# Kernel tuning notes

Hardware: AMD Instinct MI355X
Metric: run time of the kernel (lower is better)

## Reference

```python
import jax, jax.numpy as jnp
import numpy as np

B, N, C, D = 8, 8192, 3, 64
S, K = 2048, 32
EPS = 1e-7       # acos clamp epsilon (matches torch code)
BN_EPS = 1e-5    # torch BatchNorm2d default eps


def _safe_unit(v):
    # v: [..., C]; returns (v/||v|| with 0 where ||v||==0, ||v||).
    # Matches torch's `u[u != u] = 0` NaN fix and has zero grad at v==0.
    sq = jnp.sum(v * v, axis=-1, keepdims=True)
    d = jnp.where(sq > 0, jnp.sqrt(jnp.where(sq > 0, sq, 1.0)), 0.0)
    u = jnp.where(d > 0, v / jnp.where(d > 0, d, 1.0), 0.0)
    return u, d


def _acos_clamped(x):
    return jnp.arccos(jnp.clip(x, -1.0 + EPS, 1.0 - EPS))


def _conv_bn_relu(x, w, b, gamma, beta):
    # x: [B, Cin, K, S]; w: [Cout, Cin] (1x1 Conv2d); BN in training mode (batch stats).
    y = jnp.einsum('oc,bcks->boks', w, x) + b[None, :, None, None]
    mean = jnp.mean(y, axis=(0, 2, 3), keepdims=True)
    var = jnp.mean((y - mean) ** 2, axis=(0, 2, 3), keepdims=True)
    y = (y - mean) / jnp.sqrt(var + BN_EPS)
    y = y * gamma[None, :, None, None] + beta[None, :, None, None]
    return jax.nn.relu(y)


def _forward(contour, LOA, feature_maps,
             fe_w1, fe_b1, fe_g1, fe_be1, fe_w2, fe_b2, fe_g2, fe_be2,
             fl_w1, fl_b1, fl_g1, fl_be1, fl_w2, fl_b2, fl_g2, fl_be2):
    # --- downsampling: uniform linspace indices (torch .long() truncates) ---
    new_index = jnp.linspace(0.0, N - 1, S).astype(jnp.int32)               # [S]
    sampled = contour[:, new_index, :]                                       # [B,S,C]
    new_LOA = LOA[:, new_index, :]                                           # [B,S,C]
    # --- contiguous circular neighborhoods around each sampled index ---
    group_idx = (new_index[:, None] - K // 2 + jnp.arange(K)[None, :]) % N   # [S,K]
    # --- irregular gathers ---
    nb_pts = contour[:, group_idx, :]                                        # [B,S,K,C]
    nb_loa = LOA[:, group_idx, :]                                            # [B,S,K,C]
    local = nb_pts - sampled[:, :, None, :]                                  # [B,S,K,C]
    d1_unit, d1 = _safe_unit(local)
    axis = new_LOA[:, :, None, :]                                            # [B,S,1,C]
    a1 = jnp.sum(d1_unit * axis, axis=-1, keepdims=True)
    a2 = jnp.sum(d1_unit * nb_loa, axis=-1, keepdims=True)
    a3 = _acos_clamped(jnp.sum(nb_loa * axis, axis=-1, keepdims=True))
    # NOTE: torch does `D_0[D_0 == 0] = -1` on a *bool* tensor; bool(-1) is True,
    # so D_0 becomes all-True and D_0.float()*a3 == a3 (sign is always +1).
    inner_vec = local - jnp.roll(local, 1, axis=2)
    inner_unit, _ = _safe_unit(inner_vec)
    a4 = jnp.sum(inner_unit * nb_loa, axis=-1, keepdims=True)
    a5 = jnp.sum(inner_unit * jnp.roll(nb_loa, 1, axis=2), axis=-1, keepdims=True)
    a6 = _acos_clamped(jnp.sum(nb_loa * jnp.roll(nb_loa, 1, axis=2), axis=-1, keepdims=True))
    # same bool-assignment quirk for D_1 -> a6 unchanged
    d2 = _acos_clamped(jnp.sum(d1_unit * jnp.roll(d1_unit, 1, axis=2), axis=-1, keepdims=True))
    rif = jnp.concatenate([d1, d2, a1, a2, a3, a4, a5, a6], axis=-1)         # [B,S,K,8]
    # --- feature enhancement MLP on [B, ch, K, S] layout ---
    x = jnp.transpose(rif, (0, 3, 2, 1))                                     # [B,8,K,S]
    x = _conv_bn_relu(x, fe_w1, fe_b1, fe_g1, fe_be1)                        # [B,32,K,S]
    x = _conv_bn_relu(x, fe_w2, fe_b2, fe_g2, fe_be2)                        # [B,64,K,S]
    # --- gather input feature maps with the same indices, concat channels ---
    fmap = jnp.transpose(feature_maps, (0, 2, 1))                            # [B,N,D]
    grouped = jnp.transpose(fmap[:, group_idx, :], (0, 3, 2, 1))             # [B,D,K,S]
    x = jnp.concatenate([x, grouped], axis=1)                                # [B,128,K,S]
    # --- filter MLP + max over neighborhood ---
    x = _conv_bn_relu(x, fl_w1, fl_b1, fl_g1, fl_be1)                        # [B,128,K,S]
    x = _conv_bn_relu(x, fl_w2, fl_b2, fl_g2, fl_be2)                        # [B,256,K,S]
    out = jnp.max(x, axis=2)                                                 # [B,256,S]
    return sampled, new_LOA, out


def setup_inputs() -> dict:
    key = jax.random.key(0)
    ks = jax.random.split(key, 12)

    def w(k, o, i):
        return jax.random.normal(k, (o, i), jnp.float32) / np.sqrt(i)

    return {
        'contour': jax.random.normal(ks[0], (B, N, C), jnp.float32),
        'LOA': jax.random.normal(ks[1], (B, N, C), jnp.float32),
        'feature_maps': jax.random.normal(ks[2], (B, D, N), jnp.float32),
        'fe_w1': w(ks[3], 32, 8),  'fe_b1': jnp.zeros(32),
        'fe_g1': jnp.ones(32),     'fe_be1': jnp.zeros(32),
        'fe_w2': w(ks[4], 64, 32), 'fe_b2': jnp.zeros(64),
        'fe_g2': jnp.ones(64),     'fe_be2': jnp.zeros(64),
        'fl_w1': w(ks[5], 128, 128), 'fl_b1': jnp.zeros(128),
        'fl_g1': jnp.ones(128),      'fl_be1': jnp.zeros(128),
        'fl_w2': w(ks[6], 256, 128), 'fl_b2': jnp.zeros(256),
        'fl_g2': jnp.ones(256),      'fl_be2': jnp.zeros(256),
    }


def reference(contour, LOA, feature_maps,
              fe_w1, fe_b1, fe_g1, fe_be1, fe_w2, fe_b2, fe_g2, fe_be2,
              fl_w1, fl_b1, fl_g1, fl_be1, fl_w2, fl_b2, fl_g2, fl_be2):
    return _forward(contour, LOA, feature_maps,
                    fe_w1, fe_b1, fe_g1, fe_be1, fe_w2, fe_b2, fe_g2, fe_be2,
                    fl_w1, fl_b1, fl_g1, fl_be1, fl_w2, fl_b2, fl_g2, fl_be2)
```

## Files before the change

kernel.cpp:

```cpp
#include <hip/hip_runtime.h>
#include <stdint.h>

#define NPTS 8192
#define SSZ  2048
#define QTOT (8*2048*32)

#define F_MOM1   4
#define F_MOM2   12
#define F_SC1    972
#define F_SH1    1004
#define F_SC2    1036
#define F_SH2    1100
#define F_SC3    1164
#define F_SH3    1292
#define F_SC4    1420
#define F_SH4    1676
#define F_WF1    1932
#define F_WF2    2188
#define F_G1     53388
#define F_BE1    53420
#define F_G2     53452
#define F_BE2    53516
#define F_G3     53580
#define F_BE3    53708
#define F_G4     53836
#define F_BE4    54092
#define F_M1     57344
#define F_M2     57376
#define F_P      60000
#define F_S3P    77000
#define F_C4P    94000
#define CTR_OFF  524288ull
#define LOA_OFF  1310720ull
#define U3H_OFF  2097152ull
#define U3L_OFF  2129920ull
#define U4H_OFF  2162688ull
#define U4L_OFF  2228224ull
#define U2H_OFF  2293760ull
#define U2L_OFF  2297856ull
#define Y3_OFF   2301952ull
#define WS_T1    (2301952ull + 134217728ull)

typedef __attribute__((ext_vector_type(8))) short s8v;
typedef __attribute__((ext_vector_type(4))) short s4v;
typedef __attribute__((ext_vector_type(4))) float f4v;
typedef __attribute__((ext_vector_type(4))) float fl4;
#define MFMA(a,b,c) __builtin_amdgcn_mfma_f32_16x16x32_bf16(a,b,c,0,0,0)

__device__ inline float bf2f(unsigned short u){ return __uint_as_float(((uint32_t)u)<<16); }
__device__ inline unsigned short f2bf(float f){
    uint32_t x=__float_as_uint(f);
    return (unsigned short)((x + 0x7fffu + ((x>>16)&1u))>>16);
}
__device__ inline float clipf(float x){
    const float LO=(float)(-1.0+1e-7), HI=(float)(1.0-1e-7);
    return fminf(fmaxf(x,LO),HI);
}
__device__ inline float wredsum(float v){
#pragma unroll
    for(int m=1;m<64;m<<=1) v+=__shfl_xor(v,m,64);
    return v;
}
__device__ inline float ldin(const void* p,size_t i,int md){
    return md ? ((const float*)p)[i] : bf2f(((const unsigned short*)p)[i]);
}
__device__ inline int sidx(int s){ return (s*8191)/2047; }

__global__ void k_detect(const void* contour,int* flag){
    __shared__ int he;
    if(threadIdx.x==0) he=0;
    __syncthreads();
    const unsigned short* u=(const unsigned short*)contour;
    int h=0;
    for(int i=threadIdx.x;i<4096;i+=256){
        unsigned short lo=u[2*i];
        if(((lo>>7)&0xFF)>=0x86) h++;
    }
    atomicAdd(&he,h);
    __syncthreads();
    if(threadIdx.x==0) *flag = (he>400) ? 1 : 0;
}

__global__ __launch_bounds__(256) void k_convert(
    const void* ctr,const void* loa,
    const void* w1,const void* w2,const void* w3,const void* w4,
    const void* g1,const void* be1,const void* g2,const void* be2,
    const void* g3,const void* be3,const void* g4,const void* be4,
    float* F, float* ctrf, float* loaf,
    unsigned short* u2h, unsigned short* u2l,
    unsigned short* u3h, unsigned short* u3l,
    unsigned short* u4h, unsigned short* u4l,
    float* out)
{
    int md=((const int*)F)[0];
    int i = blockIdx.x*256+threadIdx.x;
    ctrf[i]=ldin(ctr,i,md);
    loaf[i]=ldin(loa,i,md);
    if(i<16384){
        int b=i>>11, s=i&2047;
        int idx=sidx(s);
        size_t cb=((size_t)b*NPTS+idx)*3;
        size_t ob=(size_t)i*3;
        out[ob]        =ldin(ctr,cb  ,md);
        out[ob+1]      =ldin(ctr,cb+1,md);
        out[ob+2]      =ldin(ctr,cb+2,md);
        out[49152+ob]  =ldin(loa,cb  ,md);
        out[49152+ob+1]=ldin(loa,cb+1,md);
        out[49152+ob+2]=ldin(loa,cb+2,md);
    }
    if(i<256)  F[F_WF1+i]=ldin(w1,i,md);
    if(i<2048) F[F_WF2+i]=ldin(w2,i,md);
    if(i<2048){
        int j=i&7, lane=(i>>3)&63, mt=i>>9;
        int m=lane&15, kk=((lane>>4)<<3)|j;
        float w=ldin(w2,(size_t)(mt*16+m)*32 + kk, md);
        unsigned short hi=f2bf(w);
        u2h[i]=hi; u2l[i]=f2bf(w-bf2f(hi));
    }
    if(i<16384){
        int j=i&7, lane=(i>>3)&63, kt=(i>>9)&3, mt=i>>11;
        int m=lane&15, kk=((lane>>4)<<3)|j;
        float w=ldin(w3,(size_t)(mt*16+m)*128 + kt*32+kk, md);
        unsigned short hi=f2bf(w);
        u3h[i]=hi; u3l[i]=f2bf(w-bf2f(hi));
    }
    if(i<32768){
        int j=i&7, lane=(i>>3)&63, kt=(i>>9)&3, mt=i>>11;
        int m=lane&15, kk=((lane>>4)<<3)|j;
        float w=ldin(w4,(size_t)(mt*16+m)*128 + kt*32+kk, md);
        unsigned short hi=f2bf(w);
        u4h[i]=hi; u4l[i]=f2bf(w-bf2f(hi));
    }
    if(i<968)   F[4+i]=0.f;
    if(i<16896) F[F_P+i]=0.f;
    if(i<16384) F[F_S3P+i]=0.f;
    if(i<32768) F[F_C4P+i]=0.f;
    if(i<32){ F[F_G1+i]=ldin(g1,i,md); F[F_BE1+i]=ldin(be1,i,md); }
    if(i<64){ F[F_G2+i]=ldin(g2,i,md); F[F_BE2+i]=ldin(be2,i,md); }
    if(i<128){ F[F_G3+i]=ldin(g3,i,md); F[F_BE3+i]=ldin(be3,i,md); }
    if(i<256){ F[F_G4+i]=ldin(g4,i,md); F[F_BE4+i]=ldin(be4,i,md); }
}

__device__ inline void rif_compute(const float* __restrict__ ctr,const float* __restrict__ loa,
                                   int b,int s,int k,float r[8])
{
    int idx=sidx(s);
    int gi=(idx-16+k)&(NPTS-1);
    size_t cb=((size_t)b*NPTS+gi)*3;
    float px=ctr[cb],py=ctr[cb+1],pz=ctr[cb+2];
    float lx=loa[cb],ly=loa[cb+1],lz=loa[cb+2];
    float sx=__shfl(px,16,32),sy=__shfl(py,16,32),sz=__shfl(pz,16,32);
    float ax=__shfl(lx,16,32),ay=__shfl(ly,16,32),az=__shfl(lz,16,32);
    float vx=px-sx,vy=py-sy,vz=pz-sz;
    float sq=vx*vx+vy*vy+vz*vz;
    float d1=sq>0.f?sqrtf(sq):0.f;
    float inv=d1>0.f?1.f/d1:0.f;
    float ux=vx*inv,uy=vy*inv,uz=vz*inv;
    float a1=ux*ax+uy*ay+uz*az;
    float a2=ux*lx+uy*ly+uz*lz;
    float a3=acosf(clipf(lx*ax+ly*ay+lz*az));
    int src=(k+31)&31;
    float pvx=__shfl(vx,src,32),pvy=__shfl(vy,src,32),pvz=__shfl(vz,src,32);
    float plx=__shfl(lx,src,32),ply=__shfl(ly,src,32),plz=__shfl(lz,src,32);
    float pux=__shfl(ux,src,32),puy=__shfl(uy,src,32),puz=__shfl(uz,src,32);
    float ivx=vx-pvx,ivy=vy-pvy,ivz=vz-pvz;
    float isq=ivx*ivx+ivy*ivy+ivz*ivz;
    float idn=isq>0.f?1.f/sqrtf(isq):0.f;
    float iux=ivx*idn,iuy=ivy*idn,iuz=ivz*idn;
    float a4=iux*lx+iuy*ly+iuz*lz;
    float a5=iux*plx+iuy*ply+iuz*plz;
    float a6=acosf(clipf(lx*plx+ly*ply+lz*plz));
    float d2=acosf(clipf(ux*pux+uy*puy+uz*puz));
    r[0]=d1;r[1]=d2;r[2]=a1;r[3]=a2;r[4]=a3;r[5]=a4;r[6]=a5;r[7]=a6;
}

__global__ __launch_bounds__(256) void k_features(
    const float* __restrict__ ctrf,const float* __restrict__ loaf,
    float* __restrict__ mom1,float* __restrict__ mom2)
{
    __shared__ float sm1[8],sm2[64];
    int t=threadIdx.x;
    if(t<8)sm1[t]=0.f;
    if(t<64)sm2[t]=0.f;
    __syncthreads();
    int lane=t&63,k=t&31;
    int q=blockIdx.x*256+t;
    int pos=q>>5,b=pos>>11,s=pos&2047;
    float r[8];
    rif_compute(ctrf,loaf,b,s,k,r);
#pragma unroll
    for(int i=0;i<8;i++){ float sv=wredsum(r[i]); if(lane==0)atomicAdd(&sm1[i],sv); }
#pragma unroll
    for(int i=0;i<8;i++)
#pragma unroll
        for(int j=i;j<8;j++){ float sv=wredsum(r[i]*r[j]); if(lane==0)atomicAdd(&sm2[i*8+j],sv); }
    __syncthreads();
    if(t<8)atomicAdd(&mom1[t],sm1[t]);
    if(t<64)atomicAdd(&mom2[t],sm2[t]);
}

__global__ void k_bn1(float* F){
    int o=threadIdx.x;
    if(o>=32)return;
    const float invP=1.0f/(float)QTOT;
    float m[8],w[8];
#pragma unroll
    for(int c=0;c<8;c++){ m[c]=F[F_MOM1+c]*invP; w[c]=F[F_WF1+o*8+c]; }
    float Ey=0.f;
#pragma unroll
    for(int c=0;c<8;c++) Ey+=w[c]*m[c];
    float Eyy=0.f;
#pragma unroll
    for(int i=0;i<8;i++)
#pragma unroll
        for(int j=0;j<8;j++){
            int a=i<j?i:j,bb=i<j?j:i;
            Eyy+=w[i]*w[j]*F[F_MOM2+a*8+bb]*invP;
        }
    float var=fmaxf(Eyy-Ey*Ey,0.f);
    float sc=F[F_G1+o]/sqrtf(var+1e-5f);
    F[F_SC1+o]=sc;
    F[F_SH1+o]=F[F_BE1+o]-Ey*sc;
}

#define S2T 264
__global__ __launch_bounds__(256) void k_stats2m(
    const float* __restrict__ ctrf,const float* __restrict__ loaf,
    const float* __restrict__ F,float* __restrict__ P)
{
    __shared__ unsigned short TH[32*S2T];
    __shared__ unsigned short TL[32*S2T];
    int t=threadIdx.x, wv=t>>6, lane=t&63;
    int quad=lane>>4, col=lane&15;
    int mi=wv>>1, ni=wv&1;
    float acc8[8];
#pragma unroll
    for(int k=0;k<8;k++) acc8[k]=0.f;
    f4v Z; Z[0]=0.f;Z[1]=0.f;Z[2]=0.f;Z[3]=0.f;
    f4v C0=Z, C1=Z;
    const float* wf1=F+F_WF1;
    const float* sc1=F+F_SC1; const float* sh1=F+F_SH1;
    for(int tt=0;tt<2;++tt){
        int tile=blockIdx.x*2+tt;
        int pos=tile*8 + wv*2 + (lane>>5);
        int b=pos>>11, s=pos&2047;
        float r[8]; rif_compute(ctrf,loaf,b,s,lane&31,r);
        int mypos=wv*64+lane;
#pragma unroll
        for(int c=0;c<32;c++){
            const float* w=wf1+c*8;
            float y=w[0]*r[0]+w[1]*r[1]+w[2]*r[2]+w[3]*r[3]
                   +w[4]*r[4]+w[5]*r[5]+w[6]*r[6]+w[7]*r[7];
            float h=fmaxf(y*sc1[c]+sh1[c],0.f);
            unsigned short hi=f2bf(h);
            TH[c*S2T+mypos]=hi;
            TL[c*S2T+mypos]=f2bf(h-bf2f(hi));
        }
        __syncthreads();
#pragma unroll
        for(int kt=0;kt<8;kt++){
            s8v AH=*(const s8v*)(TH+(mi*16+col)*S2T + kt*32 + quad*8);
            s8v AL=*(const s8v*)(TL+(mi*16+col)*S2T + kt*32 + quad*8);
            s8v BH=*(const s8v*)(TH+(ni*16+col)*S2T + kt*32 + quad*8);
            s8v BL=*(const s8v*)(TL+(ni*16+col)*S2T + kt*32 + quad*8);
            if(kt&1){
                C1=MFMA(AH,BH,C1); C1=MFMA(AH,BL,C1); C1=MFMA(AL,BH,C1);
            }else{
                C0=MFMA(AH,BH,C0); C0=MFMA(AH,BL,C0); C0=MFMA(AL,BH,C0);
            }
        }
#pragma unroll
        for(int k=0;k<8;k++){
            int c=wv*8+k;
            const unsigned short* ph=TH+c*S2T+lane*4;
            const unsigned short* pl=TL+c*S2T+lane*4;
            acc8[k]+=bf2f(ph[0])+bf2f(ph[1])+bf2f(ph[2])+bf2f(ph[3])
                    +bf2f(pl[0])+bf2f(pl[1])+bf2f(pl[2])+bf2f(pl[3]);
        }
        __syncthreads();
    }
    float* Ps=P+(size_t)(blockIdx.x&15)*1056;
#pragma unroll
    for(int rg=0;rg<4;rg++){
        float v=C0[rg]+C1[rg];
        atomicAdd(&Ps[32+(mi*16+quad*4+rg)*32 + ni*16+col], v);
    }
#pragma unroll
    for(int k=0;k<8;k++){
        float sv=wredsum(acc8[k]);
        if(lane==0) atomicAdd(&Ps[wv*8+k],sv);
    }
}

__global__ void k_red(float* F){
    int t=threadIdx.x;
    for(int e=t;e<1056;e+=256){
        float s=0.f;
#pragma unroll
        for(int k=0;k<16;k++) s+=F[F_P+k*1056+e];
        if(e<32) F[F_M1+e]=s; else F[F_M2+e-32]=s;
    }
    __syncthreads();
    int o=t;
    if(o<64){
        const float invP=1.0f/(float)QTOT;
        const float* w=F+F_WF2+o*32;
        const float* M2=F+F_M2;
        float Ey=0.f;
#pragma unroll
        for(int c=0;c<32;c++) Ey+=w[c]*F[F_M1+c];
        Ey*=invP;
        float Eyy=0.f;
        for(int c1=0;c1<32;c1++){
            float acc=0.f;
#pragma unroll
            for(int c2=0;c2<32;c2++) acc+=w[c2]*M2[c1*32+c2];
            Eyy+=w[c1]*acc;
        }
        Eyy*=invP;
        float var=fmaxf(Eyy-Ey*Ey,0.f);
        float s=F[F_G2+o]/sqrtf(var+1e-5f);
        F[F_SC2+o]=s;
        F[F_SH2+o]=F[F_BE2+o]-Ey*s;
    }
}

__global__ void k_bnd3(float* F){
    int o=threadIdx.x;
    if(o>=128)return;
    float sum=0.f,ssq=0.f;
    for(int s=0;s<64;s++){
        sum+=F[F_S3P+s*256+o];
        ssq+=F[F_S3P+s*256+128+o];
    }
    const float invP=1.0f/(float)QTOT;
    float mean=sum*invP;
    float var=fmaxf(ssq*invP-mean*mean,0.f);
    float sc=F[F_G3+o]/sqrtf(var+1e-5f);
    F[F_SC3+o]=sc;
    F[F_SH3+o]=F[F_BE3+o]-mean*sc;
}

__global__ void k_bnd4(float* F){
    int o=threadIdx.x;
    if(o>=256)return;
    float sum=0.f,ssq=0.f;
    for(int s=0;s<64;s++){
        sum+=F[F_C4P+s*512+o];
        ssq+=F[F_C4P+s*512+256+o];
    }
    const float invP=1.0f/(float)QTOT;
    float mean=sum*invP;
    float var=fmaxf(ssq*invP-mean*mean,0.f);
    float sc=F[F_G4+o]/sqrtf(var+1e-5f);
    F[F_SC4+o]=sc;
    F[F_SH4+o]=F[F_BE4+o]-mean*sc;
}

#define XST 136

__device__ inline void build_x2_8(
    const float* __restrict__ ctrf,const float* __restrict__ loaf,
    const void* __restrict__ fm,const float* __restrict__ F,
    const unsigned short* __restrict__ u2h,const unsigned short* __restrict__ u2l,
    int md,int b,int s0,int wv,int lane,
    unsigned short* XH,unsigned short* XL)
{
    int quad=lane>>4, col=lane&15;
    if(wv<4){
        float r8[8]; rif_compute(ctrf,loaf,b,s0+(lane>>5),lane&31,r8);
        const float* wf1=F+F_WF1;
        const float* sc1=F+F_SC1; const float* sh1=F+F_SH1;
        s8v vh,vl;
#pragma unroll
        for(int j=0;j<8;j++){
            int o=8*wv+j;
            const float* w=wf1+o*8;
            float y=w[0]*r8[0]+w[1]*r8[1]+w[2]*r8[2]+w[3]*r8[3]
                   +w[4]*r8[4]+w[5]*r8[5]+w[6]*r8[6]+w[7]*r8[7];
            float h=fmaxf(y*sc1[o]+sh1[o],0.f);
            unsigned short hi=f2bf(h);
            vh[j]=(short)hi;
            vl[j]=(short)f2bf(h-bf2f(hi));
        }
        *(s8v*)(XH + lane*XST + 8*wv)=vh;
        *(s8v*)(XL + lane*XST + 8*wv)=vl;
    }else{
        int dbase=16*(wv-4);
        int s=s0+(lane>>5), k=lane&31;
        int gi=(sidx(s)-16+k)&(NPTS-1);
        size_t fb=(size_t)b*64*NPTS+gi;
        for(int g=0;g<2;g++){
            s8v vh,vl;
#pragma unroll
            for(int j=0;j<8;j++){
                int d=dbase+g*8+j;
                float v = md ? ((const float*)fm)[fb+(size_t)d*NPTS]
                             : bf2f(((const unsigned short*)fm)[fb+(size_t)d*NPTS]);
                unsigned short hi=f2bf(v);
                vh[j]=(short)hi;
                vl[j]=(short)f2bf(v-bf2f(hi));
            }
            *(s8v*)(XH + lane*XST + 64 + dbase + g*8)=vh;
            *(s8v*)(XL + lane*XST + 64 + dbase + g*8)=vl;
        }
    }
    __syncthreads();
    int cg=wv>>1, nb=(wv&1)*2;
    s8v AH=*(const s8v*)(u2h+(cg*64+lane)*8);
    s8v AL=*(const s8v*)(u2l+(cg*64+lane)*8);
    s8v BH0=*(const s8v*)(XH+((nb  )*16+col)*XST+quad*8);
    s8v BL0=*(const s8v*)(XL+((nb  )*16+col)*XST+quad*8);
    s8v BH1=*(const s8v*)(XH+((nb+1)*16+col)*XST+quad*8);
    s8v BL1=*(const s8v*)(XL+((nb+1)*16+col)*XST+quad*8);
    f4v Z; Z[0]=0.f;Z[1]=0.f;Z[2]=0.f;Z[3]=0.f;
    f4v c0=MFMA(AH,BH0,Z), c1=MFMA(AH,BH1,Z);
    c0=MFMA(AH,BL0,c0); c1=MFMA(AH,BL1,c1);
    c0=MFMA(AL,BH0,c0); c1=MFMA(AL,BH1,c1);
    __syncthreads();
    const float* sc2=F+F_SC2; const float* sh2=F+F_SH2;
    int chb=cg*16+quad*4;
    float g0=sc2[chb],g1=sc2[chb+1],g2=sc2[chb+2],g3=sc2[chb+3];
    float b0=sh2[chb],b1=sh2[chb+1],b2=sh2[chb+2],b3=sh2[chb+3];
#pragma unroll
    for(int i=0;i<2;i++){
        f4v c = i? c1 : c0;
        int p=(nb+i)*16+col;
        float v0=fmaxf(c[0]*g0+b0,0.f);
        float v1=fmaxf(c[1]*g1+b1,0.f);
        float v2=fmaxf(c[2]*g2+b2,0.f);
        float v3=fmaxf(c[3]*g3+b3,0.f);
        unsigned short h0=f2bf(v0),h1=f2bf(v1),h2=f2bf(v2),h3=f2bf(v3);
        s4v vh,vl;
        vh[0]=(short)h0; vh[1]=(short)h1; vh[2]=(short)h2; vh[3]=(short)h3;
        vl[0]=(short)f2bf(v0-bf2f(h0)); vl[1]=(short)f2bf(v1-bf2f(h1));
        vl[2]=(short)f2bf(v2-bf2f(h2)); vl[3]=(short)f2bf(v3-bf2f(h3));
        *(s4v*)(XH + p*XST + chb)=vh;
        *(s4v*)(XL + p*XST + chb)=vl;
    }
}

#define G1_STEP8(UH,UL) \
    for(int kt=0;kt<4;kt++){ \
        s8v BH[4],BL[4]; \
        for(int nt=0;nt<4;nt++){ \
            int boff=(nt*16+col)*XST + kt*32 + quad*8; \
            BH[nt]=*(const s8v*)(XH+boff); \
            BL[nt]=*(const s8v*)(XL+boff); \
        } \
        { \
            s8v AH=*(const s8v*)(UH+((wv*4+kt)*64+lane)*8); \
            s8v AL=*(const s8v*)(UL+((wv*4+kt)*64+lane)*8); \
            for(int nt=0;nt<4;nt++) C[nt]=MFMA(AH,BH[nt],C[nt]); \
            for(int nt=0;nt<4;nt++) C[nt]=MFMA(AH,BL[nt],C[nt]); \
            for(int nt=0;nt<4;nt++) C[nt]=MFMA(AL,BH[nt],C[nt]); \
        } \
    }

#define G2_STEP8(UH,UL) \
    for(int kt=0;kt<4;kt++){ \
        s8v BH[4],BL[4]; \
        for(int nt=0;nt<4;nt++){ \
            int boff=(nt*16+col)*XST + kt*32 + quad*8; \
            BH[nt]=*(const s8v*)(XH+boff); \
            BL[nt]=*(const s8v*)(XL+boff); \
        } \
        for(int mi=0;mi<2;mi++){ \
            int mt=2*wv+mi; \
            s8v AH=*(const s8v*)(UH+((mt*4+kt)*64+lane)*8); \
            s8v AL=*(const s8v*)(UL+((mt*4+kt)*64+lane)*8); \
            for(int nt=0;nt<4;nt++) C2[mi][nt]=MFMA(AH,BH[nt],C2[mi][nt]); \
            for(int nt=0;nt<4;nt++) C2[mi][nt]=MFMA(AH,BL[nt],C2[mi][nt]); \
            for(int nt=0;nt<4;nt++) C2[mi][nt]=MFMA(AL,BH[nt],C2[mi][nt]); \
        } \
    }

__global__ __launch_bounds__(512) void k_stats3(
    const float* __restrict__ ctrf,const float* __restrict__ loaf,
    const void* __restrict__ fm,float* __restrict__ F,
    const unsigned short* __restrict__ u2h,const unsigned short* __restrict__ u2l,
    const unsigned short* __restrict__ u3h,const unsigned short* __restrict__ u3l,
    unsigned short* __restrict__ y3)
{
    __shared__ unsigned short XH[64*XST];
    __shared__ unsigned short XL[64*XST];
    __shared__ float as_[128],qs_[128];
    int t=threadIdx.x, wv=t>>6, lane=t&63;
    if(t<128){as_[t]=0.f;qs_[t]=0.f;}
    int md=((const int*)F)[0];
    int pos0=blockIdx.x*2, b=pos0>>11, s0=pos0&2047;
    build_x2_8(ctrf,loaf,fm,F,u2h,u2l,md,b,s0,wv,lane,XH,XL);
    __syncthreads();
    int quad=lane>>4, col=lane&15;
    f4v Z; Z[0]=0.f;Z[1]=0.f;Z[2]=0.f;Z[3]=0.f;
    f4v C[4];
#pragma unroll
    for(int nt=0;nt<4;nt++) C[nt]=Z;
#pragma unroll
    G1_STEP8(u3h,u3l)
    if(y3){
#pragma unroll
        for(int nt=0;nt<4;nt++){
            s4v v4;
#pragma unroll
            for(int rg=0;rg<4;rg++) v4[rg]=(short)f2bf(C[nt][rg]);
            *(s4v*)(y3 + (size_t)blockIdx.x*8192 + (size_t)(wv*4+nt)*256 + lane*4) = v4;
        }
    }
#pragma unroll
    for(int rg=0;rg<4;rg++){
        float sm=0.f,sq=0.f;
#pragma unroll
        for(int nt=0;nt<4;nt++){ float v=C[nt][rg]; sm+=v; sq+=v*v; }
        sm+=__shfl_xor(sm,1); sq+=__shfl_xor(sq,1);
        sm+=__shfl_xor(sm,2); sq+=__shfl_xor(sq,2);
        sm+=__shfl_xor(sm,4); sq+=__shfl_xor(sq,4);
        sm+=__shfl_xor(sm,8); sq+=__shfl_xor(sq,8);
        if(col==0){
            int ch=wv*16+quad*4+rg;
            atomicAdd(&as_[ch],sm); atomicAdd(&qs_[ch],sq);
        }
    }
    __syncthreads();
    float* Ps=F+F_S3P+(size_t)(blockIdx.x&63)*256;
    if(t<128){atomicAdd(&Ps[t],as_[t]);atomicAdd(&Ps[128+t],qs_[t]);}
}

__global__ __launch_bounds__(512) void k_conv4y(
    float* __restrict__ F,
    const unsigned short* __restrict__ u4h,const unsigned short* __restrict__ u4l,
    const unsigned short* __restrict__ y3,
    float* __restrict__ maxb)
{
    __shared__ unsigned short XH[64*XST];
    __shared__ unsigned short XL[64*XST];
    __shared__ float as_[256],qs_[256];
    int t=threadIdx.x, wv=t>>6, lane=t&63;
    if(t<256){as_[t]=0.f; qs_[t]=0.f;}
    int quad=lane>>4, col=lane&15;
    int pos0=blockIdx.x*2, b=pos0>>11, s0=pos0&2047;
    const float* sc3=F+F_SC3; const float* sh3=F+F_SH3;
    {
        int chb=wv*16+quad*4;
#pragma unroll
        for(int nt=0;nt<4;nt++){
            s4v v4=*(const s4v*)(y3 + (size_t)blockIdx.x*8192 + (size_t)(wv*4+nt)*256 + lane*4);
            s4v vh,vl;
#pragma unroll
            for(int rg=0;rg<4;rg++){
                float v=bf2f((unsigned short)v4[rg]);
                v=fmaxf(v*sc3[chb+rg]+sh3[chb+rg],0.f);
                unsigned short hi=f2bf(v);
                vh[rg]=(short)hi;
                vl[rg]=(short)f2bf(v-bf2f(hi));
            }
            int p=nt*16+col;
            *(s4v*)(XH + p*XST + chb)=vh;
            *(s4v*)(XL + p*XST + chb)=vl;
        }
    }
    __syncthreads();
    f4v Z; Z[0]=0.f;Z[1]=0.f;Z[2]=0.f;Z[3]=0.f;
    f4v C2[2][4];
#pragma unroll
    for(int mi=0;mi<2;mi++)
#pragma unroll
        for(int nt=0;nt<4;nt++) C2[mi][nt]=Z;
#pragma unroll
    G2_STEP8(u4h,u4l)
#pragma unroll
    for(int mi=0;mi<2;mi++){
        int mt=2*wv+mi;
#pragma unroll
        for(int rg=0;rg<4;rg++){
            float sm=0.f,sq=0.f,mx0=-3.4e38f,mx1=-3.4e38f;
#pragma unroll
            for(int nt=0;nt<4;nt++){
                float v=C2[mi][nt][rg];
                sm+=v; sq+=v*v;
                if(nt<2) mx0=fmaxf(mx0,v); else mx1=fmaxf(mx1,v);
            }
            sm+=__shfl_xor(sm,1); sq+=__shfl_xor(sq,1);
            sm+=__shfl_xor(sm,2); sq+=__shfl_xor(sq,2);
            sm+=__shfl_xor(sm,4); sq+=__shfl_xor(sq,4);
            sm+=__shfl_xor(sm,8); sq+=__shfl_xor(sq,8);
            mx0=fmaxf(mx0,__shfl_xor(mx0,1)); mx1=fmaxf(mx1,__shfl_xor(mx1,1));
            mx0=fmaxf(mx0,__shfl_xor(mx0,2)); mx1=fmaxf(mx1,__shfl_xor(mx1,2));
            mx0=fmaxf(mx0,__shfl_xor(mx0,4)); mx1=fmaxf(mx1,__shfl_xor(mx1,4));
            mx0=fmaxf(mx0,__shfl_xor(mx0,8)); mx1=fmaxf(mx1,__shfl_xor(mx1,8));
            if(col==0){
                int ch=mt*16+quad*4+rg;
                atomicAdd(&as_[ch],sm); atomicAdd(&qs_[ch],sq);
                size_t ob=((size_t)b*256+ch)*SSZ + s0;
                maxb[ob]=mx0; maxb[ob+1]=mx1;
            }
        }
    }
    __syncthreads();
    float* Ps=F+F_C4P+(size_t)(blockIdx.x&63)*512;
    if(t<256){atomicAdd(&Ps[t],as_[t]);atomicAdd(&Ps[256+t],qs_[t]);}
}

__global__ __launch_bounds__(512) void k_conv4(
    const float* __restrict__ ctrf,const float* __restrict__ loaf,
    const void* __restrict__ fm,float* __restrict__ F,
    const unsigned short* __restrict__ u2h,const unsigned short* __restrict__ u2l,
    const unsigned short* __restrict__ u3h,const unsigned short* __restrict__ u3l,
    const unsigned short* __restrict__ u4h,const unsigned short* __restrict__ u4l,
    float* __restrict__ maxb)
{
    __shared__ unsigned short XH[64*XST];
    __shared__ unsigned short XL[64*XST];
    __shared__ float as_[256],qs_[256];
    int t=threadIdx.x, wv=t>>6, lane=t&63;
    if(t<256){as_[t]=0.f; qs_[t]=0.f;}
    int md=((const int*)F)[0];
    int pos0=blockIdx.x*2, b=pos0>>11, s0=pos0&2047;
    build_x2_8(ctrf,loaf,fm,F,u2h,u2l,md,b,s0,wv,lane,XH,XL);
    __syncthreads();
    int quad=lane>>4, col=lane&15;
    f4v Z; Z[0]=0.f;Z[1]=0.f;Z[2]=0.f;Z[3]=0.f;
    f4v C[4];
#pragma unroll
    for(int nt=0;nt<4;nt++) C[nt]=Z;
#pragma unroll
    G1_STEP8(u3h,u3l)
    __syncthreads();
    const float* sc3=F+F_SC3; const float* sh3=F+F_SH3;
    {
        int chb=wv*16+quad*4;
#pragma unroll
        for(int nt=0;nt<4;nt++){
            int p=nt*16+col;
            s4v vh,vl;
#pragma unroll
            for(int rg=0;rg<4;rg++){
                float v=C[nt][rg];
                v=fmaxf(v*sc3[chb+rg]+sh3[chb+rg],0.f);
                unsigned short hi=f2bf(v);
                vh[rg]=(short)hi;
                vl[rg]=(short)f2bf(v-bf2f(hi));
            }
            *(s4v*)(XH + p*XST + chb)=vh;
            *(s4v*)(XL + p*XST + chb)=vl;
        }
    }
    __syncthreads();
    f4v C2[2][4];
#pragma unroll
    for(int mi=0;mi<2;mi++)
#pragma unroll
        for(int nt=0;nt<4;nt++) C2[mi][nt]=Z;
#pragma unroll
    G2_STEP8(u4h,u4l)
#pragma unroll
    for(int mi=0;mi<2;mi++){
        int mt=2*wv+mi;
#pragma unroll
        for(int rg=0;rg<4;rg++){
            float sm=0.f,sq=0.f,mx0=-3.4e38f,mx1=-3.4e38f;
#pragma unroll
            for(int nt=0;nt<4;nt++){
                float v=C2[mi][nt][rg];
                sm+=v; sq+=v*v;
                if(nt<2) mx0=fmaxf(mx0,v); else mx1=fmaxf(mx1,v);
            }
            sm+=__shfl_xor(sm,1); sq+=__shfl_xor(sq,1);
            sm+=__shfl_xor(sm,2); sq+=__shfl_xor(sq,2);
            sm+=__shfl_xor(sm,4); sq+=__shfl_xor(sq,4);
            sm+=__shfl_xor(sm,8); sq+=__shfl_xor(sq,8);
            mx0=fmaxf(mx0,__shfl_xor(mx0,1)); mx1=fmaxf(mx1,__shfl_xor(mx1,1));
            mx0=fmaxf(mx0,__shfl_xor(mx0,2)); mx1=fmaxf(mx1,__shfl_xor(mx1,2));
            mx0=fmaxf(mx0,__shfl_xor(mx0,4)); mx1=fmaxf(mx1,__shfl_xor(mx1,4));
            mx0=fmaxf(mx0,__shfl_xor(mx0,8)); mx1=fmaxf(mx1,__shfl_xor(mx1,8));
            if(col==0){
                int ch=mt*16+quad*4+rg;
                atomicAdd(&as_[ch],sm); atomicAdd(&qs_[ch],sq);
                size_t ob=((size_t)b*256+ch)*SSZ + s0;
                maxb[ob]=mx0; maxb[ob+1]=mx1;
            }
        }
    }
    __syncthreads();
    float* Ps=F+F_C4P+(size_t)(blockIdx.x&63)*512;
    if(t<256){atomicAdd(&Ps[t],as_[t]);atomicAdd(&Ps[256+t],qs_[t]);}
}

__global__ __launch_bounds__(256) void k_apply(
    const float* __restrict__ F,float* __restrict__ out)
{
    int e4=blockIdx.x*256+threadIdx.x;
    int j=(e4>>9)&255;
    float sc=F[F_SC4+j],sh=F[F_SH4+j];
    fl4* p=(fl4*)(out+98304)+e4;
    fl4 v=*p;
    v[0]=fmaxf(v[0]*sc+sh,0.f);
    v[1]=fmaxf(v[1]*sc+sh,0.f);
    v[2]=fmaxf(v[2]*sc+sh,0.f);
    v[3]=fmaxf(v[3]*sc+sh,0.f);
    *p=v;
}

extern "C" void kernel_launch(void* const* d_in, const int* in_sizes, int n_in,
                              void* d_out, int out_size, void* d_ws, size_t ws_size,
                              hipStream_t stream)
{
    const void* contour=d_in[0];
    const void* loa    =d_in[1];
    const void* fm     =d_in[2];
    const void* w1 =d_in[3];  const void* g1 =d_in[5];  const void* be1=d_in[6];
    const void* w2 =d_in[7];  const void* g2 =d_in[9];  const void* be2=d_in[10];
    const void* w3 =d_in[11]; const void* g3 =d_in[13]; const void* be3=d_in[14];
    const void* w4 =d_in[15]; const void* g4 =d_in[17]; const void* be4=d_in[18];
    float* out=(float*)d_out;

    float* F=(float*)d_ws;
    char* base=(char*)d_ws;
    float* ctrf=(float*)(base+CTR_OFF);
    float* loaf=(float*)(base+LOA_OFF);
    unsigned short* u3h=(unsigned short*)(base+U3H_OFF);
    unsigned short* u3l=(unsigned short*)(base+U3L_OFF);
    unsigned short* u4h=(unsigned short*)(base+U4H_OFF);
    unsigned short* u4l=(unsigned short*)(base+U4L_OFF);
    unsigned short* u2h=(unsigned short*)(base+U2H_OFF);
    unsigned short* u2l=(unsigned short*)(base+U2L_OFF);
    int tier = (ws_size >= WS_T1) ? 1 : 0;
    unsigned short* y3 = tier==1 ? (unsigned short*)(base+Y3_OFF) : (unsigned short*)0;
    float* maxb=out+98304;

    k_detect<<<1,256,0,stream>>>(contour,(int*)d_ws);
    k_convert<<<768,256,0,stream>>>(contour,loa,w1,w2,w3,w4,g1,be1,g2,be2,g3,be3,g4,be4,
                                    F,ctrf,loaf,u2h,u2l,u3h,u3l,u4h,u4l,out);
    k_features<<<2048,256,0,stream>>>(ctrf,loaf,F+F_MOM1,F+F_MOM2);
    k_bn1<<<1,32,0,stream>>>(F);
    k_stats2m<<<1024,256,0,stream>>>(ctrf,loaf,F,F+F_P);
    k_red<<<1,256,0,stream>>>(F);
    k_stats3<<<8192,512,0,stream>>>(ctrf,loaf,fm,F,u2h,u2l,u3h,u3l,y3);
    k_bnd3<<<1,128,0,stream>>>(F);
    if(tier==1){
        k_conv4y<<<8192,512,0,stream>>>(F,u4h,u4l,y3,maxb);
    }else{
        k_conv4<<<8192,512,0,stream>>>(ctrf,loaf,fm,F,u2h,u2l,u3h,u3l,u4h,u4l,maxb);
    }
    k_bnd4<<<1,256,0,stream>>>(F);
    k_apply<<<4096,256,0,stream>>>(F,out);
}
```

Measured before the change: 591.5 us.

## Cache per-neighbor geometric features in workspace and reuse across stats kernels

k_features now writes its 8 per-neighbor rotation-invariant features into a workspace buffer when the workspace is large enough. k_stats2m and a new k_stats3r variant read that buffer instead of recomputing the acos-heavy features, so the trigonometry runs once instead of three times. The cost is 16 MB of extra writes and reads, and this path only runs when the workspace exceeds the new tier threshold.

After: 531.3 us. -10.2%, faster.

```diff
diff --git a/kernel.cpp b/kernel.cpp
--- a/kernel.cpp
+++ b/kernel.cpp
@@ -40,6 +40,8 @@
 #define U2L_OFF  2297856ull
 #define Y3_OFF   2301952ull
 #define WS_T1    (2301952ull + 134217728ull)
+#define R_OFF    (2301952ull + 134217728ull)
+#define WS_T2    (R_OFF + 16777216ull)
 
 typedef __attribute__((ext_vector_type(8))) short s8v;
 typedef __attribute__((ext_vector_type(4))) short s4v;
@@ -176,7 +178,8 @@
 
 __global__ __launch_bounds__(256) void k_features(
     const float* __restrict__ ctrf,const float* __restrict__ loaf,
-    float* __restrict__ mom1,float* __restrict__ mom2)
+    float* __restrict__ mom1,float* __restrict__ mom2,
+    float* __restrict__ rbuf)
 {
     __shared__ float sm1[8],sm2[64];
     int t=threadIdx.x;
@@ -188,6 +191,12 @@
     int pos=q>>5,b=pos>>11,s=pos&2047;
     float r[8];
     rif_compute(ctrf,loaf,b,s,k,r);
+    if(rbuf){
+        fl4 a; a[0]=r[0];a[1]=r[1];a[2]=r[2];a[3]=r[3];
+        fl4 c; c[0]=r[4];c[1]=r[5];c[2]=r[6];c[3]=r[7];
+        ((fl4*)rbuf)[(size_t)q*2  ]=a;
+        ((fl4*)rbuf)[(size_t)q*2+1]=c;
+    }
 #pragma unroll
     for(int i=0;i<8;i++){ float sv=wredsum(r[i]); if(lane==0)atomicAdd(&sm1[i],sv); }
 #pragma unroll
@@ -226,7 +235,8 @@
 #define S2T 264
 __global__ __launch_bounds__(256) void k_stats2m(
     const float* __restrict__ ctrf,const float* __restrict__ loaf,
-    const float* __restrict__ F,float* __restrict__ P)
+    const float* __restrict__ F,float* __restrict__ P,
+    const float* __restrict__ rbuf)
 {
     __shared__ unsigned short TH[32*S2T];
     __shared__ unsigned short TL[32*S2T];
@@ -244,7 +254,15 @@
         int tile=blockIdx.x*2+tt;
         int pos=tile*8 + wv*2 + (lane>>5);
         int b=pos>>11, s=pos&2047;
-        float r[8]; rif_compute(ctrf,loaf,b,s,lane&31,r);
+        float r[8];
+        if(rbuf){
+            size_t q=((size_t)pos*32+(lane&31));
+            fl4 ra=((const fl4*)rbuf)[q*2], rc=((const fl4*)rbuf)[q*2+1];
+            r[0]=ra[0];r[1]=ra[1];r[2]=ra[2];r[3]=ra[3];
+            r[4]=rc[0];r[5]=rc[1];r[6]=rc[2];r[7]=rc[3];
+        }else{
+            rif_compute(ctrf,loaf,b,s,lane&31,r);
+        }
         int mypos=wv*64+lane;
 #pragma unroll
         for(int c=0;c<32;c++){
@@ -475,6 +493,30 @@
         } \
     }
 
+#define S3_TAIL \
+    if(y3){ \
+        for(int nt=0;nt<4;nt++){ \
+            s4v v4; \
+            for(int rg=0;rg<4;rg++) v4[rg]=(short)f2bf(C[nt][rg]); \
+            *(s4v*)(y3 + (size_t)blockIdx.x*8192 + (size_t)(wv*4+nt)*256 + lane*4) = v4; \
+        } \
+    } \
+    for(int rg=0;rg<4;rg++){ \
+        float sm=0.f,sq=0.f; \
+        for(int nt=0;nt<4;nt++){ float v=C[nt][rg]; sm+=v; sq+=v*v; } \
+        sm+=__shfl_xor(sm,1); sq+=__shfl_xor(sq,1); \
+        sm+=__shfl_xor(sm,2); sq+=__shfl_xor(sq,2); \
+        sm+=__shfl_xor(sm,4); sq+=__shfl_xor(sq,4); \
+        sm+=__shfl_xor(sm,8); sq+=__shfl_xor(sq,8); \
+        if(col==0){ \
+            int ch=wv*16+quad*4+rg; \
+            atomicAdd(&as_[ch],sm); atomicAdd(&qs_[ch],sq); \
+        } \
+    } \
+    __syncthreads(); \
+    float* Ps=F+F_S3P+(size_t)(blockIdx.x&63)*256; \
+    if(t<128){atomicAdd(&Ps[t],as_[t]);atomicAdd(&Ps[128+t],qs_[t]);}
+
 __global__ __launch_bounds__(512) void k_stats3(
     const float* __restrict__ ctrf,const float* __restrict__ loaf,
     const void* __restrict__ fm,float* __restrict__ F,
@@ -498,32 +540,105 @@
     for(int nt=0;nt<4;nt++) C[nt]=Z;
 #pragma unroll
     G1_STEP8(u3h,u3l)
-    if(y3){
-#pragma unroll
-        for(int nt=0;nt<4;nt++){
-            s4v v4;
-#pragma unroll
-            for(int rg=0;rg<4;rg++) v4[rg]=(short)f2bf(C[nt][rg]);
-            *(s4v*)(y3 + (size_t)blockIdx.x*8192 + (size_t)(wv*4+nt)*256 + lane*4) = v4;
-        }
-    }
-#pragma unroll
-    for(int rg=0;rg<4;rg++){
-        float sm=0.f,sq=0.f;
-#pragma unroll
-        for(int nt=0;nt<4;nt++){ float v=C[nt][rg]; sm+=v; sq+=v*v; }
-        sm+=__shfl_xor(sm,1); sq+=__shfl_xor(sq,1);
-        sm+=__shfl_xor(sm,2); sq+=__shfl_xor(sq,2);
-        sm+=__shfl_xor(sm,4); sq+=__shfl_xor(sq,4);
-        sm+=__shfl_xor(sm,8); sq+=__shfl_xor(sq,8);
-        if(col==0){
-            int ch=wv*16+quad*4+rg;
-            atomicAdd(&as_[ch],sm); atomicAdd(&qs_[ch],sq);
-        }
-    }
-    __syncthreads();
-    float* Ps=F+F_S3P+(size_t)(blockIdx.x&63)*256;
-    if(t<128){atomicAdd(&Ps[t],as_[t]);atomicAdd(&Ps[128+t],qs_[t]);}
+    S3_TAIL
+}
+
+__global__ __launch_bounds__(512) void k_stats3r(
+    const void* __restrict__ fm,float* __restrict__ F,
+    const float* __restrict__ rbuf,
+    const unsigned short* __restrict__ u2h,const unsigned short* __restrict__ u2l,
+    const unsigned short* __restrict__ u3h,const unsigned short* __restrict__ u3l,
+    unsigned short* __restrict__ y3)
+{
+    __shared__ unsigned short XH[64*XST];
+    __shared__ unsigned short XL[64*XST];
+    __shared__ float as_[128],qs_[128];
+    int t=threadIdx.x, wv=t>>6, lane=t&63;
+    if(t<128){as_[t]=0.f;qs_[t]=0.f;}
+    int md=((const int*)F)[0];
+    int pos0=blockIdx.x*2, b=pos0>>11, s0=pos0&2047;
+    int quad=lane>>4, col=lane&15;
+    int scol=lane>>5, k=lane&31;
+    int s=s0+scol;
+    {
+        int dbase=8*wv;
+        int gi=(sidx(s)-16+k)&(NPTS-1);
+        size_t fb=(size_t)b*64*NPTS+gi;
+        s8v fvh,fvl;
+#pragma unroll
+        for(int j=0;j<8;j++){
+            int d=dbase+j;
+            float v = md ? ((const float*)fm)[fb+(size_t)d*NPTS]
+                         : bf2f(((const unsigned short*)fm)[fb+(size_t)d*NPTS]);
+            unsigned short hi=f2bf(v);
+            fvh[j]=(short)hi;
+            fvl[j]=(short)f2bf(v-bf2f(hi));
+        }
+        *(s8v*)(XH + lane*XST + 64 + dbase)=fvh;
+        *(s8v*)(XL + lane*XST + 64 + dbase)=fvl;
+    }
+    {
+        size_t q=(((size_t)b*2048+s)*32+k);
+        fl4 ra=((const fl4*)rbuf)[q*2], rc=((const fl4*)rbuf)[q*2+1];
+        const float* wf1=F+F_WF1;
+        const float* sc1=F+F_SC1; const float* sh1=F+F_SH1;
+        s4v vh,vl;
+#pragma unroll
+        for(int j=0;j<4;j++){
+            int o=wv*4+j;
+            const float* w=wf1+o*8;
+            float y=w[0]*ra[0]+w[1]*ra[1]+w[2]*ra[2]+w[3]*ra[3]
+                   +w[4]*rc[0]+w[5]*rc[1]+w[6]*rc[2]+w[7]*rc[3];
+            float h=fmaxf(y*sc1[o]+sh1[o],0.f);
+            unsigned short hi=f2bf(h);
+            vh[j]=(short)hi;
+            vl[j]=(short)f2bf(h-bf2f(hi));
+        }
+        *(s4v*)(XH + lane*XST + wv*4)=vh;
+        *(s4v*)(XL + lane*XST + wv*4)=vl;
+    }
+    __syncthreads();
+    int cg=wv>>1, nb=(wv&1)*2;
+    s8v AH=*(const s8v*)(u2h+(cg*64+lane)*8);
+    s8v AL=*(const s8v*)(u2l+(cg*64+lane)*8);
+    s8v BH0=*(const s8v*)(XH+((nb  )*16+col)*XST+quad*8);
+    s8v BL0=*(const s8v*)(XL+((nb  )*16+col)*XST+quad*8);
+    s8v BH1=*(const s8v*)(XH+((nb+1)*16+col)*XST+quad*8);
+    s8v BL1=*(const s8v*)(XL+((nb+1)*16+col)*XST+quad*8);
+    f4v Z; Z[0]=0.f;Z[1]=0.f;Z[2]=0.f;Z[3]=0.f;
+    f4v c0=MFMA(AH,BH0,Z), c1=MFMA(AH,BH1,Z);
+    c0=MFMA(AH,BL0,c0); c1=MFMA(AH,BL1,c1);
+    c0=MFMA(AL,BH0,c0); c1=MFMA(AL,BH1,c1);
+    __syncthreads();
+    {
+        const float* sc2=F+F_SC2; const float* sh2=F+F_SH2;
+        int chb=cg*16+quad*4;
+        float g0=sc2[chb],g1=sc2[chb+1],g2=sc2[chb+2],g3=sc2[chb+3];
+        float b0=sh2[chb],b1=sh2[chb+1],b2=sh2[chb+2],b3=sh2[chb+3];
+#pragma unroll
+        for(int i=0;i<2;i++){
+            f4v c = i? c1 : c0;
+            int p=(nb+i)*16+col;
+            float v0=fmaxf(c[0]*g0+b0,0.f);
+            float v1=fmaxf(c[1]*g1+b1,0.f);
+            float v2=fmaxf(c[2]*g2+b2,0.f);
+            float v3=fmaxf(c[3]*g3+b3,0.f);
+            unsigned short h0=f2bf(v0),h1=f2bf(v1),h2=f2bf(v2),h3=f2bf(v3);
+            s4v vh,vl;
+            vh[0]=(short)h0; vh[1]=(short)h1; vh[2]=(short)h2; vh[3]=(short)h3;
+            vl[0]=(short)f2bf(v0-bf2f(h0)); vl[1]=(short)f2bf(v1-bf2f(h1));
+            vl[2]=(short)f2bf(v2-bf2f(h2)); vl[3]=(short)f2bf(v3-bf2f(h3));
+            *(s4v*)(XH + p*XST + chb)=vh;
+            *(s4v*)(XL + p*XST + chb)=vl;
+        }
+    }
+    __syncthreads();
+    f4v C[4];
+#pragma unroll
+    for(int nt=0;nt<4;nt++) C[nt]=Z;
+#pragma unroll
+    G1_STEP8(u3h,u3l)
+    S3_TAIL
 }
 
 __global__ __launch_bounds__(512) void k_conv4y(
@@ -724,20 +839,25 @@
     unsigned short* u4l=(unsigned short*)(base+U4L_OFF);
     unsigned short* u2h=(unsigned short*)(base+U2H_OFF);
     unsigned short* u2l=(unsigned short*)(base+U2L_OFF);
-    int tier = (ws_size >= WS_T1) ? 1 : 0;
-    unsigned short* y3 = tier==1 ? (unsigned short*)(base+Y3_OFF) : (unsigned short*)0;
+    int tier = (ws_size >= WS_T2) ? 2 : (ws_size >= WS_T1) ? 1 : 0;
+    unsigned short* y3 = tier>=1 ? (unsigned short*)(base+Y3_OFF) : (unsigned short*)0;
+    float* rbuf = tier==2 ? (float*)(base+R_OFF) : (float*)0;
     float* maxb=out+98304;
 
     k_detect<<<1,256,0,stream>>>(contour,(int*)d_ws);
     k_convert<<<768,256,0,stream>>>(contour,loa,w1,w2,w3,w4,g1,be1,g2,be2,g3,be3,g4,be4,
                                     F,ctrf,loaf,u2h,u2l,u3h,u3l,u4h,u4l,out);
-    k_features<<<2048,256,0,stream>>>(ctrf,loaf,F+F_MOM1,F+F_MOM2);
+    k_features<<<2048,256,0,stream>>>(ctrf,loaf,F+F_MOM1,F+F_MOM2,rbuf);
     k_bn1<<<1,32,0,stream>>>(F);
-    k_stats2m<<<1024,256,0,stream>>>(ctrf,loaf,F,F+F_P);
+    k_stats2m<<<1024,256,0,stream>>>(ctrf,loaf,F,F+F_P,rbuf);
     k_red<<<1,256,0,stream>>>(F);
-    k_stats3<<<8192,512,0,stream>>>(ctrf,loaf,fm,F,u2h,u2l,u3h,u3l,y3);
+    if(tier==2){
+        k_stats3r<<<8192,512,0,stream>>>(fm,F,rbuf,u2h,u2l,u3h,u3l,y3);
+    }else{
+        k_stats3<<<8192,512,0,stream>>>(ctrf,loaf,fm,F,u2h,u2l,u3h,u3l,y3);
+    }
     k_bnd3<<<1,128,0,stream>>>(F);
-    if(tier==1){
+    if(tier>=1){
         k_conv4y<<<8192,512,0,stream>>>(F,u4h,u4l,y3,maxb);
     }else{
         k_conv4<<<8192,512,0,stream>>>(ctrf,loaf,fm,F,u2h,u2l,u3h,u3l,u4h,u4l,maxb);
```
